# Optimization experiments

Hardware: AMD Instinct MI355X
Metric: run time of the kernel (lower is better)

## Reference

```python
import jax, jax.numpy as jnp
import numpy as np
import math

BATCH = 8192
INPUT_DIM = 4096
N_FEATURES = 2048
HAD = 4096  # 2**ceil(log2(max(input_dim, n_features)))
SCALE = math.sqrt(2.0 / N_FEATURES)
INV_SQRT_HAD = 1.0 / math.sqrt(HAD)


def fwht(x):
    """Fast Walsh-Hadamard transform, exact replica of the torch butterfly.
    x: [B, HAD] -> [B, HAD], scaled by 1/sqrt(HAD)."""
    B = x.shape[0]
    h = 1
    while h < HAD:  # log2(HAD) iterations, fixed at trace time
        x = x.reshape(B, -1, h, 2)
        x = jnp.concatenate([x[..., 0] + x[..., 1], x[..., 0] - x[..., 1]], axis=-1)
        x = x.reshape(B, -1)
        h *= 2
    return x * INV_SQRT_HAD


def setup_inputs() -> dict:
    key = jax.random.key(0)
    kx, k1, k2, k3, kp, kb = jax.random.split(key, 6)
    x = jax.random.normal(kx, (BATCH, INPUT_DIM), dtype=jnp.float32)
    D1 = jnp.sign(jax.random.normal(k1, (HAD,), dtype=jnp.float32))
    D2 = jnp.sign(jax.random.normal(k2, (HAD,), dtype=jnp.float32))
    D3 = jnp.sign(jax.random.normal(k3, (HAD,), dtype=jnp.float32))
    perm = jax.random.permutation(kp, HAD)
    bias = jax.random.uniform(kb, (N_FEATURES,), dtype=jnp.float32) * (2.0 * math.pi)
    return {"x": x, "D1": D1, "D2": D2, "D3": D3, "bias": bias, "perm": perm}


def reference(x, D1, D2, D3, bias, perm):
    # pad to hadamard_dim if needed (no-op here since INPUT_DIM == HAD)
    if x.shape[1] < HAD:
        x = jnp.pad(x, ((0, 0), (0, HAD - x.shape[1])))
    x = x * D1
    x = fwht(x)
    x = x * D2
    x = fwht(x)
    x = x * D3
    x = x[:, perm]          # random permutation of columns
    x = x[:, :N_FEATURES]   # keep first n_features columns
    return SCALE * jnp.cos(x + bias)
```

## Files before the change

### kernel.cpp

```cpp
#include <hip/hip_runtime.h>

#define HADN 4096
#define NFEAT 2048

typedef float floatx4 __attribute__((ext_vector_type(4)));

__device__ __host__ __forceinline__ int pi_map(int q) {
  return  (((q >> 3) & 1))
        | (((q >> 11) & 1) << 1)
        | (((q >> 7) & 1) << 2)
        | (((q >> 1) & 1) << 3)
        | (((q >> 5) & 1) << 4)
        | (((q >> 9) & 1) << 5)
        | (((q >> 0) & 1) << 6)
        | (((q >> 2) & 1) << 7)
        | (((q >> 4) & 1) << 8)
        | (((q >> 6) & 1) << 9)
        | (((q >> 8) & 1) << 10)
        | (((q >> 10) & 1) << 11);
}

__device__ __host__ __forceinline__ int pi_inv_map(int p) {
  return  (((p >> 6) & 1))
        | (((p >> 3) & 1) << 1)
        | (((p >> 7) & 1) << 2)
        | (((p >> 0) & 1) << 3)
        | (((p >> 8) & 1) << 4)
        | (((p >> 4) & 1) << 5)
        | (((p >> 9) & 1) << 6)
        | (((p >> 2) & 1) << 7)
        | (((p >> 10) & 1) << 8)
        | (((p >> 5) & 1) << 9)
        | (((p >> 11) & 1) << 10)
        | (((p >> 1) & 1) << 11);
}

__device__ __forceinline__ int swz(int p) {
  return p ^ ((((p >> 6) ^ (p >> 9)) & 7) << 2);
}

template <int BIT>
__device__ __forceinline__ void bfly(float* r) {
#pragma unroll
  for (int e = 0; e < 16; ++e) {
    if ((e & BIT) == 0) {
      const int f = e | BIT;
      const float a = r[e], b = r[f];
      r[e] = a + b;
      r[f] = a - b;
    }
  }
}

template <int CTRL>
__device__ __forceinline__ void dpp_bfly(float* r, bool upper) {
  const unsigned sm = upper ? 0x80000000u : 0u;
#pragma unroll
  for (int e = 0; e < 16; ++e) {
    const int pv = __builtin_amdgcn_update_dpp(
        0, __float_as_int(r[e]), CTRL, 0xF, 0xF, true);
    r[e] = __int_as_float(pv) + __int_as_float(__float_as_int(r[e]) ^ sm);
  }
}

__global__ __launch_bounds__(256) void srf_setup(
    const float* __restrict__ D2, const float* __restrict__ D3,
    const int* __restrict__ perm,
    unsigned* __restrict__ D2sgn, float* __restrict__ d3g,
    int* __restrict__ gidx) {
  const int i = blockIdx.x * 256 + threadIdx.x;
  if (i < HADN / 32) {
    unsigned wrd = 0;
    for (int j = 0; j < 32; ++j) {
      const int p = i * 32 + j;
      wrd |= (__float_as_uint(D2[pi_inv_map(p)]) >> 31) << j;
    }
    D2sgn[i] = wrd;
  }
  if (i < NFEAT) {
    const int j = perm[i];
    gidx[i] = swz(pi_map(pi_map(j)));
    d3g[i] = 0.0625f * D3[j];
  }
}

__global__ __launch_bounds__(256) void srf_main(
    const float* __restrict__ x, const float* __restrict__ D1,
    const unsigned* __restrict__ D2sgn, const float* __restrict__ d3g,
    const int* __restrict__ gidx, const float* __restrict__ bias,
    float* __restrict__ out) {
  __shared__ float lds[HADN];
  const int tid = threadIdx.x;
  const long row = blockIdx.x;

  const float4* x4 = (const float4*)(x + row * HADN);
#pragma unroll
  for (int k = 0; k < 4; ++k) {
    const int c4 = k * 256 + tid;
    float4 v = x4[c4];
    const int p = c4 * 4;
    const float4 d = *(const float4*)(D1 + p);
    v.x *= d.x; v.y *= d.y; v.z *= d.z; v.w *= d.w;
    *(float4*)(&lds[swz(p)]) = v;
  }
  __syncthreads();

  {
    const int l = tid & 63;
    const int w = tid >> 6;
    const int base = (((l >> 2) & 1) << 2) | ((l & 1) << 5) | (((l >> 3) & 1) << 6)
                   | (((l >> 4) & 1) << 7) | (((l >> 1) & 1) << 8)
                   | (((l >> 5) & 1) << 9) | (w << 10);
    float r[16];
#pragma unroll
    for (int g = 0; g < 4; ++g) {
      const int p = base | ((g & 1) << 3) | (((g >> 1) & 1) << 4);
      const float4 v = *(const float4*)(&lds[swz(p)]);
      r[g * 4 + 0] = v.x; r[g * 4 + 1] = v.y; r[g * 4 + 2] = v.z; r[g * 4 + 3] = v.w;
    }
    bfly<2>(r); bfly<4>(r); bfly<8>(r);
    dpp_bfly<0xB1>(r, (l & 1) != 0);
    {
      const unsigned sw2 = D2sgn[base >> 5] >> (base & 4);
#pragma unroll
      for (int e = 0; e < 16; ++e) {
        const int pos = (e & 3) | ((e & 12) << 1);
        const unsigned m = (sw2 >> pos) << 31;
        r[e] = __int_as_float(__float_as_int(r[e]) ^ m);
      }
    }
    bfly<1>(r); bfly<4>(r); bfly<8>(r);
    dpp_bfly<0x4E>(r, (l & 2) != 0);
#pragma unroll
    for (int g = 0; g < 4; ++g) {
      const int p = base | ((g & 1) << 3) | (((g >> 1) & 1) << 4);
      const float4 v = make_float4(r[g * 4 + 0], r[g * 4 + 1], r[g * 4 + 2], r[g * 4 + 3]);
      *(float4*)(&lds[swz(p)]) = v;
    }
  }
  __syncthreads();

#pragma unroll
  for (int j = 0; j < 2; ++j) {
    const int idx = j * 256 + tid;
    const int o = idx * 4;
    const int4 gi = *(const int4*)(gidx + o);
    const float4 dg = *(const float4*)(d3g + o);
    const float4 bz = *(const float4*)(bias + o);
    floatx4 res;
    res.x = 0.03125f * __cosf(lds[gi.x] * dg.x + bz.x);
    res.y = 0.03125f * __cosf(lds[gi.y] * dg.y + bz.y);
    res.z = 0.03125f * __cosf(lds[gi.z] * dg.z + bz.z);
    res.w = 0.03125f * __cosf(lds[gi.w] * dg.w + bz.w);
    __builtin_nontemporal_store(res, (floatx4*)(out + row * NFEAT + o));
  }
}

extern "C" void kernel_launch(void* const* d_in, const int* in_sizes, int n_in,
                              void* d_out, int out_size, void* d_ws, size_t ws_size,
                              hipStream_t stream) {
  const float* x    = (const float*)d_in[0];
  const float* D1   = (const float*)d_in[1];
  const float* D2   = (const float*)d_in[2];
  const float* D3   = (const float*)d_in[3];
  const float* bias = (const float*)d_in[4];
  const int*   perm = (const int*)d_in[5];
  float* out = (float*)d_out;

  unsigned* D2sgn = (unsigned*)d_ws;
  float*    d3g   = (float*)(D2sgn + 128);
  int*      gidx  = (int*)(d3g + NFEAT);

  srf_setup<<<8, 256, 0, stream>>>(D2, D3, perm, D2sgn, d3g, gidx);
  srf_main<<<8192, 256, 0, stream>>>(x, D1, D2sgn, d3g, gidx, bias, out);
}
```

Measured before the change: 42.54 us.

## Load x directly into butterfly registers, skip first LDS pass, use raw hardware cos

Each thread now loads its x and D1 elements from global memory straight into the layout used by the first register butterfly stage. This removes one LDS write, one barrier and one LDS read per row. The cosine becomes the raw hardware cos instruction, which takes its input in revolutions; D3 and bias are pre-scaled by 1/(2π) in the setup kernel so one FMA forms the argument. The gidx, dgc and bzc loads are also hoisted above the barrier. Costs: the global loads are now strided float4 reads rather than fully contiguous ones, and the hardware cos may lose accuracy for large arguments.

```diff
diff --git a/kernel.cpp b/kernel.cpp
--- a/kernel.cpp
+++ b/kernel.cpp
@@ -2,6 +2,7 @@
 
 #define HADN 4096
 #define NFEAT 2048
+#define INV2PI 0.15915494309189535f
 
 typedef float floatx4 __attribute__((ext_vector_type(4)));
 
@@ -65,9 +66,9 @@
 
 __global__ __launch_bounds__(256) void srf_setup(
     const float* __restrict__ D2, const float* __restrict__ D3,
-    const int* __restrict__ perm,
-    unsigned* __restrict__ D2sgn, float* __restrict__ d3g,
-    int* __restrict__ gidx) {
+    const int* __restrict__ perm, const float* __restrict__ bias,
+    unsigned* __restrict__ D2sgn, float* __restrict__ dgc,
+    int* __restrict__ gidx, float* __restrict__ bzc) {
   const int i = blockIdx.x * 256 + threadIdx.x;
   if (i < HADN / 32) {
     unsigned wrd = 0;
@@ -80,80 +81,78 @@
   if (i < NFEAT) {
     const int j = perm[i];
     gidx[i] = swz(pi_map(pi_map(j)));
-    d3g[i] = 0.0625f * D3[j];
+    dgc[i] = 0.0625f * INV2PI * D3[j];
+    bzc[i] = INV2PI * bias[i];
   }
 }
 
 __global__ __launch_bounds__(256) void srf_main(
     const float* __restrict__ x, const float* __restrict__ D1,
-    const unsigned* __restrict__ D2sgn, const float* __restrict__ d3g,
-    const int* __restrict__ gidx, const float* __restrict__ bias,
+    const unsigned* __restrict__ D2sgn, const float* __restrict__ dgc,
+    const int* __restrict__ gidx, const float* __restrict__ bzc,
     float* __restrict__ out) {
   __shared__ float lds[HADN];
   const int tid = threadIdx.x;
   const long row = blockIdx.x;
+  const int l = tid & 63;
+  const int w = tid >> 6;
+  const int base = (((l >> 2) & 1) << 2) | ((l & 1) << 5) | (((l >> 3) & 1) << 6)
+                 | (((l >> 4) & 1) << 7) | (((l >> 1) & 1) << 8)
+                 | (((l >> 5) & 1) << 9) | (w << 10);
 
-  const float4* x4 = (const float4*)(x + row * HADN);
+  float r[16];
+  const float* xr = x + row * HADN;
 #pragma unroll
-  for (int k = 0; k < 4; ++k) {
-    const int c4 = k * 256 + tid;
-    float4 v = x4[c4];
-    const int p = c4 * 4;
-    const float4 d = *(const float4*)(D1 + p);
-    v.x *= d.x; v.y *= d.y; v.z *= d.z; v.w *= d.w;
+  for (int g = 0; g < 4; ++g) {
+    const int p = base | ((g & 1) << 3) | (((g >> 1) & 1) << 4);
+    const float4 xv = *(const float4*)(xr + p);
+    const float4 dv = *(const float4*)(D1 + p);
+    r[g * 4 + 0] = xv.x * dv.x; r[g * 4 + 1] = xv.y * dv.y;
+    r[g * 4 + 2] = xv.z * dv.z; r[g * 4 + 3] = xv.w * dv.w;
+  }
+  const unsigned sw2 = D2sgn[base >> 5] >> (base & 4);
+
+  bfly<2>(r); bfly<4>(r); bfly<8>(r);
+  dpp_bfly<0xB1>(r, (l & 1) != 0);
+#pragma unroll
+  for (int e = 0; e < 16; ++e) {
+    const int pos = (e & 3) | ((e & 12) << 1);
+    const unsigned m = (sw2 >> pos) << 31;
+    r[e] = __int_as_float(__float_as_int(r[e]) ^ m);
+  }
+  bfly<1>(r); bfly<4>(r); bfly<8>(r);
+  dpp_bfly<0x4E>(r, (l & 2) != 0);
+
+#pragma unroll
+  for (int g = 0; g < 4; ++g) {
+    const int p = base | ((g & 1) << 3) | (((g >> 1) & 1) << 4);
+    const float4 v = make_float4(r[g * 4 + 0], r[g * 4 + 1], r[g * 4 + 2], r[g * 4 + 3]);
     *(float4*)(&lds[swz(p)]) = v;
   }
+
+  const int o0 = tid * 4;
+  const int o1 = (256 + tid) * 4;
+  const int4   gi0 = *(const int4*)(gidx + o0);
+  const float4 dg0 = *(const float4*)(dgc + o0);
+  const float4 bz0 = *(const float4*)(bzc + o0);
+  const int4   gi1 = *(const int4*)(gidx + o1);
+  const float4 dg1 = *(const float4*)(dgc + o1);
+  const float4 bz1 = *(const float4*)(bzc + o1);
   __syncthreads();
 
-  {
-    const int l = tid & 63;
-    const int w = tid >> 6;
-    const int base = (((l >> 2) & 1) << 2) | ((l & 1) << 5) | (((l >> 3) & 1) << 6)
-                   | (((l >> 4) & 1) << 7) | (((l >> 1) & 1) << 8)
-                   | (((l >> 5) & 1) << 9) | (w << 10);
-    float r[16];
-#pragma unroll
-    for (int g = 0; g < 4; ++g) {
-      const int p = base | ((g & 1) << 3) | (((g >> 1) & 1) << 4);
-      const float4 v = *(const float4*)(&lds[swz(p)]);
-      r[g * 4 + 0] = v.x; r[g * 4 + 1] = v.y; r[g * 4 + 2] = v.z; r[g * 4 + 3] = v.w;
-    }
-    bfly<2>(r); bfly<4>(r); bfly<8>(r);
-    dpp_bfly<0xB1>(r, (l & 1) != 0);
-    {
-      const unsigned sw2 = D2sgn[base >> 5] >> (base & 4);
-#pragma unroll
-      for (int e = 0; e < 16; ++e) {
-        const int pos = (e & 3) | ((e & 12) << 1);
-        const unsigned m = (sw2 >> pos) << 31;
-        r[e] = __int_as_float(__float_as_int(r[e]) ^ m);
-      }
-    }
-    bfly<1>(r); bfly<4>(r); bfly<8>(r);
-    dpp_bfly<0x4E>(r, (l & 2) != 0);
-#pragma unroll
-    for (int g = 0; g < 4; ++g) {
-      const int p = base | ((g & 1) << 3) | (((g >> 1) & 1) << 4);
-      const float4 v = make_float4(r[g * 4 + 0], r[g * 4 + 1], r[g * 4 + 2], r[g * 4 + 3]);
-      *(float4*)(&lds[swz(p)]) = v;
-    }
-  }
-  __syncthreads();
-
-#pragma unroll
-  for (int j = 0; j < 2; ++j) {
-    const int idx = j * 256 + tid;
-    const int o = idx * 4;
-    const int4 gi = *(const int4*)(gidx + o);
-    const float4 dg = *(const float4*)(d3g + o);
-    const float4 bz = *(const float4*)(bias + o);
-    floatx4 res;
-    res.x = 0.03125f * __cosf(lds[gi.x] * dg.x + bz.x);
-    res.y = 0.03125f * __cosf(lds[gi.y] * dg.y + bz.y);
-    res.z = 0.03125f * __cosf(lds[gi.z] * dg.z + bz.z);
-    res.w = 0.03125f * __cosf(lds[gi.w] * dg.w + bz.w);
-    __builtin_nontemporal_store(res, (floatx4*)(out + row * NFEAT + o));
-  }
+  float* op = out + row * NFEAT;
+  floatx4 res0;
+  res0.x = 0.03125f * __builtin_amdgcn_cosf(fmaf(lds[gi0.x], dg0.x, bz0.x));
+  res0.y = 0.03125f * __builtin_amdgcn_cosf(fmaf(lds[gi0.y], dg0.y, bz0.y));
+  res0.z = 0.03125f * __builtin_amdgcn_cosf(fmaf(lds[gi0.z], dg0.z, bz0.z));
+  res0.w = 0.03125f * __builtin_amdgcn_cosf(fmaf(lds[gi0.w], dg0.w, bz0.w));
+  __builtin_nontemporal_store(res0, (floatx4*)(op + o0));
+  floatx4 res1;
+  res1.x = 0.03125f * __builtin_amdgcn_cosf(fmaf(lds[gi1.x], dg1.x, bz1.x));
+  res1.y = 0.03125f * __builtin_amdgcn_cosf(fmaf(lds[gi1.y], dg1.y, bz1.y));
+  res1.z = 0.03125f * __builtin_amdgcn_cosf(fmaf(lds[gi1.z], dg1.z, bz1.z));
+  res1.w = 0.03125f * __builtin_amdgcn_cosf(fmaf(lds[gi1.w], dg1.w, bz1.w));
+  __builtin_nontemporal_store(res1, (floatx4*)(op + o1));
 }
 
 extern "C" void kernel_launch(void* const* d_in, const int* in_sizes, int n_in,
@@ -168,9 +167,10 @@
   float* out = (float*)d_out;
 
   unsigned* D2sgn = (unsigned*)d_ws;
-  float*    d3g   = (float*)(D2sgn + 128);
-  int*      gidx  = (int*)(d3g + NFEAT);
+  float*    dgc   = (float*)(D2sgn + 128);
+  int*      gidx  = (int*)(dgc + NFEAT);
+  float*    bzc   = (float*)(gidx + NFEAT);
 
-  srf_setup<<<8, 256, 0, stream>>>(D2, D3, perm, D2sgn, d3g, gidx);
-  srf_main<<<8192, 256, 0, stream>>>(x, D1, D2sgn, d3g, gidx, bias, out);
+  srf_setup<<<8, 256, 0, stream>>>(D2, D3, perm, bias, D2sgn, dgc, gidx, bzc);
+  srf_main<<<8192, 256, 0, stream>>>(x, D1, D2sgn, dgc, gidx, bzc, out);
 }
```

After: 50.21 us. +18.0%, slower.
